# Performance work log

Measured on AMD Instinct MI355X. Metric: run time of the kernel, lower is better.

The kernel has to match this reference:

```python
import jax, jax.numpy as jnp
from jax import lax
import numpy as np

B, C, H, W = 64, 3, 224, 224
NPARAM, NSEV, NCHROMA, K = 8, 5, 1, 37
SEVERITY = 3  # ctor default
CHROMA = 0   # random.random()*nchroma made deterministic


def setup_inputs() -> dict:
    key = jax.random.key(0)
    k1, k2, k3, k4, k5 = jax.random.split(key, 5)
    batch = jax.random.uniform(k1, (B, C, H, W), dtype=jnp.float32)
    targets = jax.random.randint(k2, (B,), 0, 1000, dtype=jnp.int32)
    psf_stack = jax.random.uniform(k3, (NPARAM, NSEV, NCHROMA, C, K, K), dtype=jnp.float32)
    params = jax.random.randint(k4, (B,), 0, NPARAM, dtype=jnp.int32)
    weights = jax.random.uniform(k5, (B,), dtype=jnp.float32)
    return {"batch": batch, "targets": targets, "psf_stack": psf_stack,
            "params": params, "weights": weights}


def reference(batch, targets, psf_stack, params, weights):
    # kernels for chosen severity/chroma: [NPARAM, C, K, K]
    kernels = psf_stack[:, SEVERITY - 1, CHROMA]
    k = kernels[params]                      # per-sample kernels [B, C, K, K]
    b, c, h, w = batch.shape
    p = K // 2
    # reflect pad (torch F.pad mode='reflect')
    xp = jnp.pad(batch, ((0, 0), (0, 0), (p, p), (p, p)), mode='reflect')
    # per-sample per-channel (depthwise) conv as one grouped conv with B*C groups
    x = xp.reshape(1, b * c, h + 2 * p, w + 2 * p)
    kw = k.reshape(b * c, 1, K, K)
    blurred = lax.conv_general_dilated(
        x, kw, window_strides=(1, 1), padding='VALID',
        feature_group_count=b * c,
        dimension_numbers=('NCHW', 'OIHW', 'NCHW'),
    ).reshape(b, c, h, w)
    wv = weights.reshape(-1, 1, 1, 1)
    out = (1.0 - wv) * batch + wv * blurred  # normalize is identity by default
    return out, targets
```

## Files before the change

### kernel.cpp

```cpp
#include <hip/hip_runtime.h>

#define BB 64
#define CC 3
#define HH 224
#define WW 224
#define KK 37
#define PP 18
#define PLANE (HH*WW)

#define BM 32
#define BROWS 68
#define BSTR 264
#define FRAGS 2560
#define NTT (8*CC*KK)

typedef __attribute__((ext_vector_type(8)))  __bf16 bf16x8;
typedef __attribute__((ext_vector_type(16))) float  f32x16;

__device__ __forceinline__ unsigned short f2bf(float f) {
    unsigned int u = __float_as_uint(f);
    return (unsigned short)((u + 0x7FFFu + ((u >> 16) & 1u)) >> 16);
}
__device__ __forceinline__ float bf2f(unsigned short h) {
    return __uint_as_float(((unsigned int)h) << 16);
}

__global__ __launch_bounds__(256) void build_frags(
    const float* __restrict__ psf, unsigned short* __restrict__ tt)
{
    const int s = blockIdx.x;
    const int ky = s % KK;
    const int pc = s / KK;
    const int p = pc / CC, c = pc - (pc / CC) * CC;
    const float* wrow = psf + (size_t)(((p*5 + 2)*CC + c)*KK + ky) * KK;
    unsigned short* dst = tt + (size_t)s * FRAGS;
    for (int e = threadIdx.x; e < FRAGS; e += 256) {
        int j = e & 7, ln = (e >> 3) & 31, hi = (e >> 8) & 1, q = e >> 9;
        int kx = 16*q + 8*hi + j - ln;
        dst[e] = (kx >= 0 && kx < KK) ? f2bf(wrow[kx]) : (unsigned short)0;
    }
}

__device__ __forceinline__ void load_bq_ws(bf16x8 (&bq)[5], const unsigned short* kybase) {
    #pragma unroll
    for (int q = 0; q < 5; ++q)
        bq[q] = *(const bf16x8*)(kybase + q*512);
}

__device__ __forceinline__ void load_bq_fb(bf16x8 (&bq)[5], const unsigned short* s_w16,
                                           int ky, int hi, int ln) {
    #pragma unroll
    for (int q = 0; q < 5; ++q) {
        union { bf16x8 v; unsigned short s[8]; } u;
        #pragma unroll
        for (int j = 0; j < 8; ++j) {
            int kx = 16*q + 8*hi + j - ln;
            u.s[j] = (kx >= 0 && kx < KK) ? s_w16[ky*40 + kx] : (unsigned short)0;
        }
        bq[q] = u.v;
    }
}

#define MFMA_(T,Q) T = __builtin_amdgcn_mfma_f32_32x32x16_bf16(af, bq[Q], T, 0, 0, 0)

template<int NT>
__device__ __forceinline__ void compute_ky(const unsigned short* rp, const bf16x8 (&bq)[5],
                                           f32x16& A0, f32x16& A1)
{
    bf16x8 af;
#define LDC(c) af = *(const bf16x8*)(rp + 16*(c))
    if constexpr (NT == 2) {
        LDC(0); MFMA_(A0,0);
        LDC(1); MFMA_(A0,1);
        LDC(2); MFMA_(A0,2); MFMA_(A1,0);
        LDC(3); MFMA_(A0,3); MFMA_(A1,1);
        LDC(4); MFMA_(A0,4); MFMA_(A1,2);
        LDC(5); MFMA_(A1,3);
        LDC(6); MFMA_(A1,4);
    } else {
        LDC(0); MFMA_(A0,0);
        LDC(1); MFMA_(A0,1);
        LDC(2); MFMA_(A0,2);
        LDC(3); MFMA_(A0,3);
        LDC(4); MFMA_(A0,4);
    }
#undef LDC
}

template<bool FROM_WS, int NT>
__device__ __forceinline__ void kloop(
    const unsigned short* base,
    const unsigned short* fb,
    int hi, int ln, f32x16& A0, f32x16& A1)
{
    bf16x8 bqA[5], bqB[5];
    if constexpr (FROM_WS) load_bq_ws(bqA, fb); else load_bq_fb(bqA, fb, 0, hi, ln);
    for (int ky = 0; ky < KK; ky += 2) {
        if (ky + 1 < KK) {
            if constexpr (FROM_WS) load_bq_ws(bqB, fb + (size_t)(ky + 1)*FRAGS);
            else load_bq_fb(bqB, fb, ky + 1, hi, ln);
        }
        __builtin_amdgcn_s_setprio(1);
        compute_ky<NT>(base + ky*BSTR, bqA, A0, A1);
        __builtin_amdgcn_s_setprio(0);
        if (ky + 1 >= KK) break;
        if (ky + 2 < KK) {
            if constexpr (FROM_WS) load_bq_ws(bqA, fb + (size_t)(ky + 2)*FRAGS);
            else load_bq_fb(bqA, fb, ky + 2, hi, ln);
        }
        __builtin_amdgcn_s_setprio(1);
        compute_ky<NT>(base + (ky + 1)*BSTR, bqB, A0, A1);
        __builtin_amdgcn_s_setprio(0);
    }
}

template<bool FROM_WS>
__global__ __launch_bounds__(256, 4) void optics_mfma(
    const float* __restrict__ batch,
    const float* __restrict__ psf,
    const unsigned short* __restrict__ tt,
    const int* __restrict__ params,
    const float* __restrict__ weights,
    float* __restrict__ out)
{
    __shared__ __align__(16) unsigned short s_band[BROWS*BSTR + 16];
    __shared__ __align__(16) unsigned short s_w16[FROM_WS ? 8 : KK*40];

    const int tid = threadIdx.x;
    const int yband = blockIdx.x;
    const int plane = blockIdx.y;
    const int b = plane / CC, c = plane - b*CC;
    const int y0 = yband * BM;
    const int p = params[b];

    const float* src = batch + (size_t)plane * PLANE;
    for (int i = tid; i < BROWS*56; i += 256) {
        int r = i / 56, g = i - r*56;
        int gy = y0 + r - PP;
        gy = gy < 0 ? -gy : (gy >= HH ? 2*HH - 2 - gy : gy);
        float4 v = *(const float4*)&src[gy*WW + 4*g];
        unsigned int lo  = f2bf(v.x) | ((unsigned int)f2bf(v.y) << 16);
        unsigned int hi2 = f2bf(v.z) | ((unsigned int)f2bf(v.w) << 16);
        unsigned int* d = (unsigned int*)&s_band[r*BSTR + PP + 4*g];
        d[0] = lo; d[1] = hi2;
    }
    for (int i = tid; i < BROWS*40; i += 256) {
        int r = i / 40, e = i - r*40;
        int col = e < PP ? e : (224 + e);
        unsigned short v = 0;
        if (col < 260) {
            int gy = y0 + r - PP;
            gy = gy < 0 ? -gy : (gy >= HH ? 2*HH - 2 - gy : gy);
            int gx = col - PP;
            gx = gx < 0 ? -gx : (gx >= WW ? 2*WW - 2 - gx : gx);
            v = f2bf(src[gy*WW + gx]);
        }
        s_band[r*BSTR + col] = v;
    }
    if (tid < 16) s_band[BROWS*BSTR + tid] = 0;
    if constexpr (!FROM_WS) {
        const float* ksrc = psf + (size_t)((p*5 + 2)*CC + c) * (KK*KK);
        for (int i = tid; i < KK*KK; i += 256) {
            int ky_ = i / KK, kx_ = i - ky_*KK;
            s_w16[ky_*40 + kx_] = f2bf(ksrc[i]);
        }
    }
    __syncthreads();

    const int lane = tid & 63;
    const int w    = tid >> 6;
    const int ln   = lane & 31;
    const int hi   = lane >> 5;

    const unsigned short* fb;
    if constexpr (FROM_WS)
        fb = tt + (size_t)((p*CC + c)*KK)*FRAGS + hi*256 + ln*8;
    else
        fb = s_w16;
    const unsigned short* base = &s_band[ln*BSTR + 64*w + 8*hi];

    f32x16 A0 = {0,0,0,0, 0,0,0,0, 0,0,0,0, 0,0,0,0};
    f32x16 A1 = A0;

    if (w < 3) kloop<FROM_WS, 2>(base, fb, hi, ln, A0, A1);
    else       kloop<FROM_WS, 1>(base, fb, hi, ln, A0, A1);

    const float wt = weights[b];
    const float w1 = 1.0f - wt;
    float* dst = out + (size_t)plane * PLANE;
#define EPI(ACC, GT) { \
    _Pragma("unroll") \
    for (int r = 0; r < 16; ++r) { \
        const int rowL = (r & 3) + 8*(r >> 2) + 4*hi; \
        const int yo = y0 + rowL; \
        const int xo = 32*(GT) + ln; \
        const float orig = bf2f(s_band[(rowL + PP)*BSTR + xo + PP]); \
        dst[yo*WW + xo] = w1*orig + wt*ACC[r]; \
    } }
    EPI(A0, 2*w)
    if (w < 3) EPI(A1, 2*w + 1)
#undef EPI
}

__global__ void copy_targets(const int* __restrict__ t, float* __restrict__ out) {
    int i = threadIdx.x;
    if (i < BB) out[i] = (float)t[i];
}

extern "C" void kernel_launch(void* const* d_in, const int* in_sizes, int n_in,
                              void* d_out, int out_size, void* d_ws, size_t ws_size,
                              hipStream_t stream) {
    const float* batch   = (const float*)d_in[0];
    const int*   targets = (const int*)d_in[1];
    const float* psf     = (const float*)d_in[2];
    const int*   params  = (const int*)d_in[3];
    const float* weights = (const float*)d_in[4];
    float* out = (float*)d_out;
    unsigned short* tt = (unsigned short*)d_ws;

    const size_t need = (size_t)NTT * FRAGS * sizeof(unsigned short);
    dim3 grid(HH / BM, BB*CC);

    if (ws_size >= need) {
        build_frags<<<NTT, 256, 0, stream>>>(psf, tt);
        optics_mfma<true><<<grid, 256, 0, stream>>>(batch, psf, tt, params, weights, out);
    } else {
        optics_mfma<false><<<grid, 256, 0, stream>>>(batch, psf, tt, params, weights, out);
    }
    copy_targets<<<1, 64, 0, stream>>>(targets, out + (size_t)BB*CC*PLANE);
}
```

Baseline: 80.22 us.

## Use persistent atomic-scheduled blocks, triple-buffer weight fragments, fold targets copy

Replaces the one-block-per-tile grid with 1024 persistent blocks that take work items from an atomic counter, zeroed by a new tiny kernel. The ky loop now keeps three sets of weight fragments in flight instead of two, to hide the latency of global loads. The targets copy moves into build_frags, which removes a separate launch. The costs are an extra zeroing launch, a barrier and atomic on every item, and more register pressure from the third buffer.

```diff
diff --git a/kernel.cpp b/kernel.cpp
--- a/kernel.cpp
+++ b/kernel.cpp
@@ -13,6 +13,8 @@
 #define BSTR 264
 #define FRAGS 2560
 #define NTT (8*CC*KK)
+#define NITEMS (BB*CC*7)
+#define TT_BYTES ((size_t)NTT * FRAGS * sizeof(unsigned short))
 
 typedef __attribute__((ext_vector_type(8)))  __bf16 bf16x8;
 typedef __attribute__((ext_vector_type(16))) float  f32x16;
@@ -25,8 +27,11 @@
     return __uint_as_float(((unsigned int)h) << 16);
 }
 
+__global__ void zero_ctr(unsigned int* ctr) { if (threadIdx.x == 0) *ctr = 0u; }
+
 __global__ __launch_bounds__(256) void build_frags(
-    const float* __restrict__ psf, unsigned short* __restrict__ tt)
+    const float* __restrict__ psf, unsigned short* __restrict__ tt,
+    const int* __restrict__ targets, float* __restrict__ tout)
 {
     const int s = blockIdx.x;
     const int ky = s % KK;
@@ -39,6 +44,7 @@
         int kx = 16*q + 8*hi + j - ln;
         dst[e] = (kx >= 0 && kx < KK) ? f2bf(wrow[kx]) : (unsigned short)0;
     }
+    if (s == 0 && threadIdx.x < BB) tout[threadIdx.x] = (float)targets[threadIdx.x];
 }
 
 __device__ __forceinline__ void load_bq_ws(bf16x8 (&bq)[5], const unsigned short* kybase) {
@@ -87,44 +93,128 @@
 #undef LDC
 }
 
+#define SP1 __builtin_amdgcn_s_setprio(1)
+#define SP0 __builtin_amdgcn_s_setprio(0)
+
 template<bool FROM_WS, int NT>
 __device__ __forceinline__ void kloop(
-    const unsigned short* base,
-    const unsigned short* fb,
+    const unsigned short* base, const unsigned short* fb,
     int hi, int ln, f32x16& A0, f32x16& A1)
 {
-    bf16x8 bqA[5], bqB[5];
-    if constexpr (FROM_WS) load_bq_ws(bqA, fb); else load_bq_fb(bqA, fb, 0, hi, ln);
-    for (int ky = 0; ky < KK; ky += 2) {
-        if (ky + 1 < KK) {
-            if constexpr (FROM_WS) load_bq_ws(bqB, fb + (size_t)(ky + 1)*FRAGS);
-            else load_bq_fb(bqB, fb, ky + 1, hi, ln);
-        }
-        __builtin_amdgcn_s_setprio(1);
-        compute_ky<NT>(base + ky*BSTR, bqA, A0, A1);
-        __builtin_amdgcn_s_setprio(0);
-        if (ky + 1 >= KK) break;
-        if (ky + 2 < KK) {
-            if constexpr (FROM_WS) load_bq_ws(bqA, fb + (size_t)(ky + 2)*FRAGS);
-            else load_bq_fb(bqA, fb, ky + 2, hi, ln);
-        }
-        __builtin_amdgcn_s_setprio(1);
-        compute_ky<NT>(base + (ky + 1)*BSTR, bqB, A0, A1);
-        __builtin_amdgcn_s_setprio(0);
-    }
-}
-
-template<bool FROM_WS>
-__global__ __launch_bounds__(256, 4) void optics_mfma(
+    bf16x8 bqA[5], bqB[5], bqC[5];
+    if constexpr (FROM_WS) { load_bq_ws(bqA, fb); load_bq_ws(bqB, fb + (size_t)FRAGS); }
+    else { load_bq_fb(bqA, fb, 0, hi, ln); load_bq_fb(bqB, fb, 1, hi, ln); }
+    int ky = 0;
+    for (; ky + 2 < KK; ky += 3) {
+        if constexpr (FROM_WS) load_bq_ws(bqC, fb + (size_t)(ky + 2)*FRAGS);
+        else load_bq_fb(bqC, fb, ky + 2, hi, ln);
+        SP1; compute_ky<NT>(base + ky*BSTR, bqA, A0, A1); SP0;
+        if (ky + 3 < KK) {
+            if constexpr (FROM_WS) load_bq_ws(bqA, fb + (size_t)(ky + 3)*FRAGS);
+            else load_bq_fb(bqA, fb, ky + 3, hi, ln);
+        }
+        SP1; compute_ky<NT>(base + (ky + 1)*BSTR, bqB, A0, A1); SP0;
+        if (ky + 4 < KK) {
+            if constexpr (FROM_WS) load_bq_ws(bqB, fb + (size_t)(ky + 4)*FRAGS);
+            else load_bq_fb(bqB, fb, ky + 4, hi, ln);
+        }
+        SP1; compute_ky<NT>(base + (ky + 2)*BSTR, bqC, A0, A1); SP0;
+    }
+    if (ky < KK) { SP1; compute_ky<NT>(base + ky*BSTR, bqA, A0, A1); SP0; }
+}
+
+__global__ __launch_bounds__(256, 4) void optics_persist(
     const float* __restrict__ batch,
-    const float* __restrict__ psf,
     const unsigned short* __restrict__ tt,
     const int* __restrict__ params,
     const float* __restrict__ weights,
+    float* __restrict__ out,
+    unsigned int* __restrict__ ctr)
+{
+    __shared__ __align__(16) unsigned short s_band[BROWS*BSTR + 16];
+    __shared__ int s_item;
+
+    const int tid  = threadIdx.x;
+    const int lane = tid & 63;
+    const int w    = tid >> 6;
+    const int ln   = lane & 31;
+    const int hi   = lane >> 5;
+
+    for (;;) {
+        if (tid == 0) s_item = (int)atomicAdd(ctr, 1u);
+        __syncthreads();
+        const int item = s_item;
+        if (item >= NITEMS) break;
+
+        const int plane = item / 7;
+        const int yband = item - plane*7;
+        const int b = plane / CC, c = plane - b*CC;
+        const int y0 = yband * BM;
+        const int p = params[b];
+
+        const float* src = batch + (size_t)plane * PLANE;
+        for (int i = tid; i < BROWS*56; i += 256) {
+            int r = i / 56, g = i - r*56;
+            int gy = y0 + r - PP;
+            gy = gy < 0 ? -gy : (gy >= HH ? 2*HH - 2 - gy : gy);
+            float4 v = *(const float4*)&src[gy*WW + 4*g];
+            unsigned int lo  = f2bf(v.x) | ((unsigned int)f2bf(v.y) << 16);
+            unsigned int hi2 = f2bf(v.z) | ((unsigned int)f2bf(v.w) << 16);
+            unsigned int* d = (unsigned int*)&s_band[r*BSTR + PP + 4*g];
+            d[0] = lo; d[1] = hi2;
+        }
+        for (int i = tid; i < BROWS*40; i += 256) {
+            int r = i / 40, e = i - r*40;
+            int col = e < PP ? e : (224 + e);
+            unsigned short v = 0;
+            if (col < 260) {
+                int gy = y0 + r - PP;
+                gy = gy < 0 ? -gy : (gy >= HH ? 2*HH - 2 - gy : gy);
+                int gx = col - PP;
+                gx = gx < 0 ? -gx : (gx >= WW ? 2*WW - 2 - gx : gx);
+                v = f2bf(src[gy*WW + gx]);
+            }
+            s_band[r*BSTR + col] = v;
+        }
+        if (tid < 16) s_band[BROWS*BSTR + tid] = 0;
+        __syncthreads();
+
+        const unsigned short* fb = tt + (size_t)((p*CC + c)*KK)*FRAGS + hi*256 + ln*8;
+        const unsigned short* base = &s_band[ln*BSTR + 64*w + 8*hi];
+
+        f32x16 A0 = {0,0,0,0, 0,0,0,0, 0,0,0,0, 0,0,0,0};
+        f32x16 A1 = A0;
+
+        if (w < 3) kloop<true, 2>(base, fb, hi, ln, A0, A1);
+        else       kloop<true, 1>(base, fb, hi, ln, A0, A1);
+
+        const float wt = weights[b];
+        const float w1 = 1.0f - wt;
+        float* dst = out + (size_t)plane * PLANE;
+#define EPI(ACC, GT) { \
+        _Pragma("unroll") \
+        for (int r = 0; r < 16; ++r) { \
+            const int rowL = (r & 3) + 8*(r >> 2) + 4*hi; \
+            const int yo = y0 + rowL; \
+            const int xo = 32*(GT) + ln; \
+            const float orig = bf2f(s_band[(rowL + PP)*BSTR + xo + PP]); \
+            dst[yo*WW + xo] = w1*orig + wt*ACC[r]; \
+        } }
+        EPI(A0, 2*w)
+        if (w < 3) EPI(A1, 2*w + 1)
+#undef EPI
+    }
+}
+
+__global__ __launch_bounds__(256, 4) void optics_fb(
+    const float* __restrict__ batch,
+    const float* __restrict__ psf,
+    const int* __restrict__ params,
+    const float* __restrict__ weights,
     float* __restrict__ out)
 {
     __shared__ __align__(16) unsigned short s_band[BROWS*BSTR + 16];
-    __shared__ __align__(16) unsigned short s_w16[FROM_WS ? 8 : KK*40];
+    __shared__ __align__(16) unsigned short s_w16[KK*40];
 
     const int tid = threadIdx.x;
     const int yband = blockIdx.x;
@@ -158,7 +248,7 @@
         s_band[r*BSTR + col] = v;
     }
     if (tid < 16) s_band[BROWS*BSTR + tid] = 0;
-    if constexpr (!FROM_WS) {
+    {
         const float* ksrc = psf + (size_t)((p*5 + 2)*CC + c) * (KK*KK);
         for (int i = tid; i < KK*KK; i += 256) {
             int ky_ = i / KK, kx_ = i - ky_*KK;
@@ -171,19 +261,12 @@
     const int w    = tid >> 6;
     const int ln   = lane & 31;
     const int hi   = lane >> 5;
-
-    const unsigned short* fb;
-    if constexpr (FROM_WS)
-        fb = tt + (size_t)((p*CC + c)*KK)*FRAGS + hi*256 + ln*8;
-    else
-        fb = s_w16;
     const unsigned short* base = &s_band[ln*BSTR + 64*w + 8*hi];
 
     f32x16 A0 = {0,0,0,0, 0,0,0,0, 0,0,0,0, 0,0,0,0};
     f32x16 A1 = A0;
-
-    if (w < 3) kloop<FROM_WS, 2>(base, fb, hi, ln, A0, A1);
-    else       kloop<FROM_WS, 1>(base, fb, hi, ln, A0, A1);
+    if (w < 3) kloop<false, 2>(base, s_w16, hi, ln, A0, A1);
+    else       kloop<false, 1>(base, s_w16, hi, ln, A0, A1);
 
     const float wt = weights[b];
     const float w1 = 1.0f - wt;
@@ -217,15 +300,16 @@
     const float* weights = (const float*)d_in[4];
     float* out = (float*)d_out;
     unsigned short* tt = (unsigned short*)d_ws;
-
-    const size_t need = (size_t)NTT * FRAGS * sizeof(unsigned short);
-    dim3 grid(HH / BM, BB*CC);
-
-    if (ws_size >= need) {
-        build_frags<<<NTT, 256, 0, stream>>>(psf, tt);
-        optics_mfma<true><<<grid, 256, 0, stream>>>(batch, psf, tt, params, weights, out);
+    unsigned int* ctr = (unsigned int*)((char*)d_ws + TT_BYTES);
+
+    if (ws_size >= TT_BYTES + 64) {
+        zero_ctr<<<1, 64, 0, stream>>>(ctr);
+        build_frags<<<NTT, 256, 0, stream>>>(psf, tt, targets,
+                                             out + (size_t)BB*CC*PLANE);
+        optics_persist<<<1024, 256, 0, stream>>>(batch, tt, params, weights, out, ctr);
     } else {
-        optics_mfma<false><<<grid, 256, 0, stream>>>(batch, psf, tt, params, weights, out);
-    }
-    copy_targets<<<1, 64, 0, stream>>>(targets, out + (size_t)BB*CC*PLANE);
-}
+        dim3 grid(HH / BM, BB*CC);
+        optics_fb<<<grid, 256, 0, stream>>>(batch, psf, params, weights, out);
+        copy_targets<<<1, 64, 0, stream>>>(targets, out + (size_t)BB*CC*PLANE);
+    }
+}
```

New measurement: 92.50 us. 15.3% more time.

## Double-buffer A fragments from LDS and fold targets copy into build kernel

Applied to the files above, without the earlier changes.

Each ky row's A fragments (7 or 5 bf16x8 vectors) are now loaded from LDS into registers one ky step ahead, alongside the existing B fragment prefetch, instead of being loaded right before each MFMA. This is meant to hide LDS latency behind MFMA work. It raises register pressure, so the occupancy hint drops from 4 to 3 blocks per CU. The targets copy also moves into build_frags, which removes one kernel launch on the workspace path.

```diff
diff --git a/kernel.cpp b/kernel.cpp
--- a/kernel.cpp
+++ b/kernel.cpp
@@ -13,6 +13,7 @@
 #define BSTR 264
 #define FRAGS 2560
 #define NTT (8*CC*KK)
+#define TT_BYTES ((size_t)NTT * FRAGS * sizeof(unsigned short))
 
 typedef __attribute__((ext_vector_type(8)))  __bf16 bf16x8;
 typedef __attribute__((ext_vector_type(16))) float  f32x16;
@@ -26,7 +27,8 @@
 }
 
 __global__ __launch_bounds__(256) void build_frags(
-    const float* __restrict__ psf, unsigned short* __restrict__ tt)
+    const float* __restrict__ psf, unsigned short* __restrict__ tt,
+    const int* __restrict__ targets, float* __restrict__ tout)
 {
     const int s = blockIdx.x;
     const int ky = s % KK;
@@ -39,6 +41,7 @@
         int kx = 16*q + 8*hi + j - ln;
         dst[e] = (kx >= 0 && kx < KK) ? f2bf(wrow[kx]) : (unsigned short)0;
     }
+    if (s == 0 && threadIdx.x < BB) tout[threadIdx.x] = (float)targets[threadIdx.x];
 }
 
 __device__ __forceinline__ void load_bq_ws(bf16x8 (&bq)[5], const unsigned short* kybase) {
@@ -61,31 +64,38 @@
     }
 }
 
-#define MFMA_(T,Q) T = __builtin_amdgcn_mfma_f32_32x32x16_bf16(af, bq[Q], T, 0, 0, 0)
-
-template<int NT>
-__device__ __forceinline__ void compute_ky(const unsigned short* rp, const bf16x8 (&bq)[5],
+template<int NC>
+__device__ __forceinline__ void load_af(bf16x8 (&af)[NC], const unsigned short* rp) {
+    #pragma unroll
+    for (int c = 0; c < NC; ++c)
+        af[c] = *(const bf16x8*)(rp + 16*c);
+}
+
+#define MFMA4(T,AF,Q) T = __builtin_amdgcn_mfma_f32_32x32x16_bf16(af[AF], bq[Q], T, 0, 0, 0)
+
+template<int NT, int NC>
+__device__ __forceinline__ void compute_ky(const bf16x8 (&af)[NC], const bf16x8 (&bq)[5],
                                            f32x16& A0, f32x16& A1)
 {
-    bf16x8 af;
-#define LDC(c) af = *(const bf16x8*)(rp + 16*(c))
     if constexpr (NT == 2) {
-        LDC(0); MFMA_(A0,0);
-        LDC(1); MFMA_(A0,1);
-        LDC(2); MFMA_(A0,2); MFMA_(A1,0);
-        LDC(3); MFMA_(A0,3); MFMA_(A1,1);
-        LDC(4); MFMA_(A0,4); MFMA_(A1,2);
-        LDC(5); MFMA_(A1,3);
-        LDC(6); MFMA_(A1,4);
+        MFMA4(A0,0,0);
+        MFMA4(A0,1,1);
+        MFMA4(A0,2,2); MFMA4(A1,2,0);
+        MFMA4(A0,3,3); MFMA4(A1,3,1);
+        MFMA4(A0,4,4); MFMA4(A1,4,2);
+        MFMA4(A1,5,3);
+        MFMA4(A1,6,4);
     } else {
-        LDC(0); MFMA_(A0,0);
-        LDC(1); MFMA_(A0,1);
-        LDC(2); MFMA_(A0,2);
-        LDC(3); MFMA_(A0,3);
-        LDC(4); MFMA_(A0,4);
-    }
-#undef LDC
-}
+        MFMA4(A0,0,0);
+        MFMA4(A0,1,1);
+        MFMA4(A0,2,2);
+        MFMA4(A0,3,3);
+        MFMA4(A0,4,4);
+    }
+}
+
+#define SP1 __builtin_amdgcn_s_setprio(1)
+#define SP0 __builtin_amdgcn_s_setprio(0)
 
 template<bool FROM_WS, int NT>
 __device__ __forceinline__ void kloop(
@@ -93,29 +103,29 @@
     const unsigned short* fb,
     int hi, int ln, f32x16& A0, f32x16& A1)
 {
-    bf16x8 bqA[5], bqB[5];
+    constexpr int NC = (NT == 2) ? 7 : 5;
+    bf16x8 afA[NC], afB[NC], bqA[5], bqB[5];
+    load_af<NC>(afA, base);
     if constexpr (FROM_WS) load_bq_ws(bqA, fb); else load_bq_fb(bqA, fb, 0, hi, ln);
     for (int ky = 0; ky < KK; ky += 2) {
         if (ky + 1 < KK) {
+            load_af<NC>(afB, base + (ky + 1)*BSTR);
             if constexpr (FROM_WS) load_bq_ws(bqB, fb + (size_t)(ky + 1)*FRAGS);
             else load_bq_fb(bqB, fb, ky + 1, hi, ln);
         }
-        __builtin_amdgcn_s_setprio(1);
-        compute_ky<NT>(base + ky*BSTR, bqA, A0, A1);
-        __builtin_amdgcn_s_setprio(0);
+        SP1; compute_ky<NT, NC>(afA, bqA, A0, A1); SP0;
         if (ky + 1 >= KK) break;
         if (ky + 2 < KK) {
+            load_af<NC>(afA, base + (ky + 2)*BSTR);
             if constexpr (FROM_WS) load_bq_ws(bqA, fb + (size_t)(ky + 2)*FRAGS);
             else load_bq_fb(bqA, fb, ky + 2, hi, ln);
         }
-        __builtin_amdgcn_s_setprio(1);
-        compute_ky<NT>(base + (ky + 1)*BSTR, bqB, A0, A1);
-        __builtin_amdgcn_s_setprio(0);
+        SP1; compute_ky<NT, NC>(afB, bqB, A0, A1); SP0;
     }
 }
 
 template<bool FROM_WS>
-__global__ __launch_bounds__(256, 4) void optics_mfma(
+__global__ __launch_bounds__(256, 3) void optics_mfma(
     const float* __restrict__ batch,
     const float* __restrict__ psf,
     const unsigned short* __restrict__ tt,
@@ -218,14 +228,14 @@
     float* out = (float*)d_out;
     unsigned short* tt = (unsigned short*)d_ws;
 
-    const size_t need = (size_t)NTT * FRAGS * sizeof(unsigned short);
     dim3 grid(HH / BM, BB*CC);
 
-    if (ws_size >= need) {
-        build_frags<<<NTT, 256, 0, stream>>>(psf, tt);
+    if (ws_size >= TT_BYTES) {
+        build_frags<<<NTT, 256, 0, stream>>>(psf, tt, targets,
+                                             out + (size_t)BB*CC*PLANE);
         optics_mfma<true><<<grid, 256, 0, stream>>>(batch, psf, tt, params, weights, out);
     } else {
         optics_mfma<false><<<grid, 256, 0, stream>>>(batch, psf, tt, params, weights, out);
-    }
-    copy_targets<<<1, 64, 0, stream>>>(targets, out + (size_t)BB*CC*PLANE);
-}
+        copy_targets<<<1, 64, 0, stream>>>(targets, out + (size_t)BB*CC*PLANE);
+    }
+}
```

Result: slower. 84.97 us (+5.9%).

## Stagger per-wave ky start, add sched barriers, fold targets copy into prep

Applied to the files above, without the earlier changes.

Each wave now walks the 37 kernel rows starting at its own offset (9*w) and wraps around. Waves therefore read different weight-fragment rows and LDS rows at the same moment, which should reduce contention on L2 and LDS. Scheduling barriers pin the prefetch of the next row's fragments ahead of the MFMAs, and the loop is partially unrolled. The targets-to-float copy is folded into the build_frags kernel to save one launch. In exchange there is extra wrap-around index arithmetic, and unroll 3 adds register pressure under the 4-blocks-per-SM launch bound.

```diff
diff --git a/kernel.cpp b/kernel.cpp
--- a/kernel.cpp
+++ b/kernel.cpp
@@ -13,8 +13,10 @@
 #define BSTR 264
 #define FRAGS 2560
 #define NTT (8*CC*KK)
+#define TT_BYTES ((size_t)NTT * FRAGS * sizeof(unsigned short))
 
 typedef __attribute__((ext_vector_type(8)))  __bf16 bf16x8;
+typedef __attribute__((ext_vector_type(4)))  unsigned int u32x4;
 typedef __attribute__((ext_vector_type(16))) float  f32x16;
 
 __device__ __forceinline__ unsigned short f2bf(float f) {
@@ -26,7 +28,8 @@
 }
 
 __global__ __launch_bounds__(256) void build_frags(
-    const float* __restrict__ psf, unsigned short* __restrict__ tt)
+    const float* __restrict__ psf, unsigned short* __restrict__ tt,
+    const int* __restrict__ targets, float* __restrict__ tout)
 {
     const int s = blockIdx.x;
     const int ky = s % KK;
@@ -39,19 +42,20 @@
         int kx = 16*q + 8*hi + j - ln;
         dst[e] = (kx >= 0 && kx < KK) ? f2bf(wrow[kx]) : (unsigned short)0;
     }
-}
-
-__device__ __forceinline__ void load_bq_ws(bf16x8 (&bq)[5], const unsigned short* kybase) {
+    if (s == 0 && threadIdx.x < BB) tout[threadIdx.x] = (float)targets[threadIdx.x];
+}
+
+__device__ __forceinline__ void load_bq_ws(u32x4 (&bq)[5], const unsigned short* kybase) {
     #pragma unroll
     for (int q = 0; q < 5; ++q)
-        bq[q] = *(const bf16x8*)(kybase + q*512);
-}
-
-__device__ __forceinline__ void load_bq_fb(bf16x8 (&bq)[5], const unsigned short* s_w16,
+        bq[q] = *(const u32x4*)(kybase + q*512);
+}
+
+__device__ __forceinline__ void load_bq_fb(u32x4 (&bq)[5], const unsigned short* s_w16,
                                            int ky, int hi, int ln) {
     #pragma unroll
     for (int q = 0; q < 5; ++q) {
-        union { bf16x8 v; unsigned short s[8]; } u;
+        union { u32x4 v; unsigned short s[8]; } u;
         #pragma unroll
         for (int j = 0; j < 8; ++j) {
             int kx = 16*q + 8*hi + j - ln;
@@ -61,14 +65,15 @@
     }
 }
 
-#define MFMA_(T,Q) T = __builtin_amdgcn_mfma_f32_32x32x16_bf16(af, bq[Q], T, 0, 0, 0)
+#define MFMA_(T,Q) T = __builtin_amdgcn_mfma_f32_32x32x16_bf16( \
+    __builtin_bit_cast(bf16x8, af), __builtin_bit_cast(bf16x8, bq[Q]), T, 0, 0, 0)
 
 template<int NT>
-__device__ __forceinline__ void compute_ky(const unsigned short* rp, const bf16x8 (&bq)[5],
+__device__ __forceinline__ void compute_ky(const unsigned short* rp, const u32x4 (&bq)[5],
                                            f32x16& A0, f32x16& A1)
 {
-    bf16x8 af;
-#define LDC(c) af = *(const bf16x8*)(rp + 16*(c))
+    u32x4 af;
+#define LDC(c) af = *(const u32x4*)(rp + 16*(c))
     if constexpr (NT == 2) {
         LDC(0); MFMA_(A0,0);
         LDC(1); MFMA_(A0,1);
@@ -87,31 +92,35 @@
 #undef LDC
 }
 
+#define SP1 __builtin_amdgcn_s_setprio(1)
+#define SP0 __builtin_amdgcn_s_setprio(0)
+#define SBAR __builtin_amdgcn_sched_barrier(0)
+
 template<bool FROM_WS, int NT>
 __device__ __forceinline__ void kloop(
     const unsigned short* base,
     const unsigned short* fb,
-    int hi, int ln, f32x16& A0, f32x16& A1)
-{
-    bf16x8 bqA[5], bqB[5];
-    if constexpr (FROM_WS) load_bq_ws(bqA, fb); else load_bq_fb(bqA, fb, 0, hi, ln);
-    for (int ky = 0; ky < KK; ky += 2) {
-        if (ky + 1 < KK) {
-            if constexpr (FROM_WS) load_bq_ws(bqB, fb + (size_t)(ky + 1)*FRAGS);
-            else load_bq_fb(bqB, fb, ky + 1, hi, ln);
-        }
-        __builtin_amdgcn_s_setprio(1);
-        compute_ky<NT>(base + ky*BSTR, bqA, A0, A1);
-        __builtin_amdgcn_s_setprio(0);
-        if (ky + 1 >= KK) break;
-        if (ky + 2 < KK) {
-            if constexpr (FROM_WS) load_bq_ws(bqA, fb + (size_t)(ky + 2)*FRAGS);
-            else load_bq_fb(bqA, fb, ky + 2, hi, ln);
-        }
-        __builtin_amdgcn_s_setprio(1);
-        compute_ky<NT>(base + (ky + 1)*BSTR, bqB, A0, A1);
-        __builtin_amdgcn_s_setprio(0);
-    }
+    int off, int hi, int ln, f32x16& A0, f32x16& A1)
+{
+    u32x4 bqA[5], bqB[5];
+    int kyA = off;
+    if constexpr (FROM_WS) load_bq_ws(bqA, fb + (size_t)kyA*FRAGS);
+    else load_bq_fb(bqA, fb, kyA, hi, ln);
+    #pragma unroll 3
+    for (int t = 0; t < KK - 1; t += 2) {
+        int kyB = kyA + 1; if (kyB == KK) kyB = 0;
+        if constexpr (FROM_WS) load_bq_ws(bqB, fb + (size_t)kyB*FRAGS);
+        else load_bq_fb(bqB, fb, kyB, hi, ln);
+        SBAR;
+        SP1; compute_ky<NT>(base + kyA*BSTR, bqA, A0, A1); SP0;
+        int kyN = kyB + 1; if (kyN == KK) kyN = 0;
+        if constexpr (FROM_WS) load_bq_ws(bqA, fb + (size_t)kyN*FRAGS);
+        else load_bq_fb(bqA, fb, kyN, hi, ln);
+        SBAR;
+        SP1; compute_ky<NT>(base + kyB*BSTR, bqB, A0, A1); SP0;
+        kyA = kyN;
+    }
+    SP1; compute_ky<NT>(base + kyA*BSTR, bqA, A0, A1); SP0;
 }
 
 template<bool FROM_WS>
@@ -171,6 +180,7 @@
     const int w    = tid >> 6;
     const int ln   = lane & 31;
     const int hi   = lane >> 5;
+    const int off  = 9 * w;
 
     const unsigned short* fb;
     if constexpr (FROM_WS)
@@ -182,8 +192,8 @@
     f32x16 A0 = {0,0,0,0, 0,0,0,0, 0,0,0,0, 0,0,0,0};
     f32x16 A1 = A0;
 
-    if (w < 3) kloop<FROM_WS, 2>(base, fb, hi, ln, A0, A1);
-    else       kloop<FROM_WS, 1>(base, fb, hi, ln, A0, A1);
+    if (w < 3) kloop<FROM_WS, 2>(base, fb, off, hi, ln, A0, A1);
+    else       kloop<FROM_WS, 1>(base, fb, off, hi, ln, A0, A1);
 
     const float wt = weights[b];
     const float w1 = 1.0f - wt;
@@ -218,14 +228,14 @@
     float* out = (float*)d_out;
     unsigned short* tt = (unsigned short*)d_ws;
 
-    const size_t need = (size_t)NTT * FRAGS * sizeof(unsigned short);
     dim3 grid(HH / BM, BB*CC);
 
-    if (ws_size >= need) {
-        build_frags<<<NTT, 256, 0, stream>>>(psf, tt);
+    if (ws_size >= TT_BYTES) {
+        build_frags<<<NTT, 256, 0, stream>>>(psf, tt, targets,
+                                             out + (size_t)BB*CC*PLANE);
         optics_mfma<true><<<grid, 256, 0, stream>>>(batch, psf, tt, params, weights, out);
     } else {
         optics_mfma<false><<<grid, 256, 0, stream>>>(batch, psf, tt, params, weights, out);
-    }
-    copy_targets<<<1, 64, 0, stream>>>(targets, out + (size_t)BB*CC*PLANE);
-}
+        copy_targets<<<1, 64, 0, stream>>>(targets, out + (size_t)BB*CC*PLANE);
+    }
+}
```

Result: slower. 82.36 us (+2.7%).
